# Kernel tuning notes

Hardware: AMD Instinct MI355X
Metric: run time of the kernel (lower is better)

Reference implementation:

```python
import jax, jax.numpy as jnp
import numpy as np

N_NODES = 50000
N_FEAT = 128
HIDDEN = 3
N_EDGES = 600000
N_POWERS = 3


def setup_inputs() -> dict:
    key = jax.random.key(0)
    ks = jax.random.split(key, 6)
    x = jax.random.normal(ks[0], (N_NODES, N_FEAT), dtype=jnp.float32)
    edge_index = jax.random.randint(ks[1], (N_POWERS, 2, N_EDGES), 0, N_NODES, dtype=jnp.int64)
    # MLP params for the 3 adjacency powers, stacked on the leading axis.
    # torch Linear(in,out) stored transposed here: y = x @ W + b.
    Wa = jax.random.normal(ks[2], (N_POWERS, N_FEAT, HIDDEN), dtype=jnp.float32) * (1.0 / np.sqrt(N_FEAT))
    ba = jax.random.normal(ks[3], (N_POWERS, HIDDEN), dtype=jnp.float32) * 0.01
    Wb = jax.random.normal(ks[4], (N_POWERS, HIDDEN, 1), dtype=jnp.float32) * (1.0 / np.sqrt(HIDDEN))
    bb = jax.random.normal(ks[5], (N_POWERS, 1), dtype=jnp.float32) * 0.01
    return {"x": x, "edge_index": edge_index, "Wa": Wa, "ba": ba, "Wb": Wb, "bb": bb}


def reference(x, edge_index, Wa, ba, Wb, bb):
    # Gather source/target node features per edge, per adjacency power.
    x_j = x[edge_index[:, 0]]          # [P, E, F]
    x_i = x[edge_index[:, 1]]          # [P, E, F]
    abs_dif = jnp.abs(x_j - x_i)       # [P, E, F]
    # Tiny per-edge MLP: Linear -> ReLU -> Linear -> Sigmoid (separate params per power).
    h = jax.nn.relu(jnp.einsum('pef,pfh->peh', abs_dif, Wa) + ba[:, None, :])  # [P, E, H]
    w = jax.nn.sigmoid(jnp.einsum('peh,pho->peo', h, Wb) + bb[:, None, :])     # [P, E, 1]
    return w[..., 0]                   # [P, E] edge weights for each power
```

## Files before the change

### kernel.cpp

```cpp
#include <hip/hip_runtime.h>
#include <math.h>

#define N_NODES 50000
#define N_FEAT  128
#define N_EDGES 600000
#define N_POWERS 3

#define PAIRS 5
#define EDGES_PER_BLK (64 * PAIRS)

#define CAP 81920
#define NBUCK 8
#define CHUNK 2048
#define NCHUNK 293

typedef _Float16 half2v __attribute__((ext_vector_type(2)));
union HU { unsigned u; half2v h; };

__device__ __forceinline__ int bucket_of(int j) { return (int)(((unsigned)j * 41u) >> 18); }

__device__ __forceinline__ unsigned long long match8(int b, bool valid) {
    const unsigned long long m0 = __ballot(b & 1);
    const unsigned long long m1 = __ballot(b & 2);
    const unsigned long long m2 = __ballot(b & 4);
    const unsigned long long vm = __ballot(valid);
    unsigned long long m = (b & 1) ? m0 : ~m0;
    m &= (b & 2) ? m1 : ~m1;
    m &= (b & 4) ? m2 : ~m2;
    return m & vm;
}

__global__ __launch_bounds__(256) void conv_x_plain(const float* __restrict__ x,
                                                    unsigned* __restrict__ xh,
                                                    const float* __restrict__ Wa,
                                                    unsigned* __restrict__ wah) {
    const int t = blockIdx.x * 256 + threadIdx.x;
    const float4* x4 = (const float4*)x;
    float4 a = x4[(size_t)t * 2];
    float4 b = x4[(size_t)t * 2 + 1];
    HU p0, p1, p2, p3;
    p0.h = half2v{(_Float16)a.x, (_Float16)a.y};
    p1.h = half2v{(_Float16)a.z, (_Float16)a.w};
    p2.h = half2v{(_Float16)b.x, (_Float16)b.y};
    p3.h = half2v{(_Float16)b.z, (_Float16)b.w};
    ((uint4*)xh)[t] = uint4{p0.u, p1.u, p2.u, p3.u};
    if (blockIdx.x == 0 && threadIdx.x < 192) {
        const int tt = threadIdx.x;
        #pragma unroll
        for (int q = 0; q < 3; ++q) {
            int idx = tt + q * 192;
            int c  = idx % 3;
            int pk = idx / 3;
            int k  = pk % 64;
            int p  = pk / 64;
            float w0 = Wa[p * 384 + (2 * k) * 3 + c];
            float w1 = Wa[p * 384 + (2 * k + 1) * 3 + c];
            HU u; u.h = half2v{(_Float16)w0, (_Float16)w1};
            wah[idx] = u.u;
        }
    }
}

__global__ __launch_bounds__(256) void hist_kernel(const int* __restrict__ edge_index,
                                                   int* __restrict__ hist) {
    __shared__ int lh[NBUCK];
    const int p = blockIdx.y, chunk = blockIdx.x;
    if (threadIdx.x < NBUCK) lh[threadIdx.x] = 0;
    __syncthreads();
    const int* ej = edge_index + (size_t)p * 2 * N_EDGES;
    const int base = chunk * CHUNK;
    const int lane = threadIdx.x & 63;
    #pragma unroll
    for (int k = 0; k < 8; ++k) {
        const int e = base + k * 256 + threadIdx.x;
        const bool valid = e < N_EDGES;
        const int j = __builtin_nontemporal_load(ej + (valid ? e : 0));
        const int b = bucket_of(j);
        const unsigned long long m = match8(b, valid);
        if (valid && lane == (int)__builtin_ctzll(m))
            atomicAdd(&lh[b], (int)__popcll(m));
    }
    __syncthreads();
    if (threadIdx.x < NBUCK)
        hist[(p * NBUCK + threadIdx.x) * NCHUNK + chunk] = lh[threadIdx.x];
}

__global__ __launch_bounds__(64) void scan_hist(int* __restrict__ hist,
                                                int* __restrict__ cur) {
    const int pb = blockIdx.x;
    const int lane = threadIdx.x;
    int* h = hist + pb * NCHUNK;
    int carry = 0;
    for (int t = 0; t < NCHUNK; t += 64) {
        const int c = t + lane;
        int v = (c < NCHUNK) ? h[c] : 0;
        int s = v;
        #pragma unroll
        for (int d = 1; d < 64; d <<= 1) {
            int u = __shfl_up(s, d, 64);
            if (lane >= d) s += u;
        }
        if (c < NCHUNK) h[c] = carry + (s - v);
        carry += __shfl(s, 63, 64);
    }
    if (lane == 0) cur[pb] = carry;
}

__global__ __launch_bounds__(256) void scatter_pass(const int* __restrict__ edge_index,
                                                    const int* __restrict__ hist,
                                                    unsigned long long* __restrict__ su) {
    __shared__ int lc[NBUCK];
    const int p = blockIdx.y, chunk = blockIdx.x;
    if (threadIdx.x < NBUCK)
        lc[threadIdx.x] = hist[(p * NBUCK + threadIdx.x) * NCHUNK + chunk];
    __syncthreads();
    const int* ej = edge_index + (size_t)p * 2 * N_EDGES;
    const int* ei = ej + N_EDGES;
    const int base = chunk * CHUNK;
    const int lane = threadIdx.x & 63;
    #pragma unroll
    for (int k = 0; k < 8; ++k) {
        const int e = base + k * 256 + threadIdx.x;
        const bool valid = e < N_EDGES;
        const int j = __builtin_nontemporal_load(ej + (valid ? e : 0));
        const int i = __builtin_nontemporal_load(ei + (valid ? e : 0));
        const int b = bucket_of(j);
        const unsigned long long m = match8(b, valid);
        const int ldr = m ? (int)__builtin_ctzll(m) : 0;
        int basepos = 0;
        if (valid && lane == ldr)
            basepos = atomicAdd(&lc[b], (int)__popcll(m));
        basepos = __shfl(basepos, ldr, 64);
        if (valid) {
            const int rank = (int)__popcll(m & ((1ull << lane) - 1ull));
            const size_t slot = (size_t)(p * NBUCK + b) * CAP + basepos + rank;
            su[slot] = (unsigned long long)(unsigned)(j | (i << 16))
                     | ((unsigned long long)e << 32);
        }
    }
}

template<int PAT>
__device__ __forceinline__ float swz(float v) {
    return __int_as_float(__builtin_amdgcn_ds_swizzle(__float_as_int(v), PAT));
}

__device__ __forceinline__ void dot3_8(const uint4& qa0, const uint4& qa1,
                                       const uint4& qb0, const uint4& qb1,
                                       const HU wa[8][3],
                                       float& h0, float& h1, float& h2) {
    unsigned ua[8] = {qa0.x, qa0.y, qa0.z, qa0.w, qa1.x, qa1.y, qa1.z, qa1.w};
    unsigned ub[8] = {qb0.x, qb0.y, qb0.z, qb0.w, qb1.x, qb1.y, qb1.z, qb1.w};
    h0 = 0.f; h1 = 0.f; h2 = 0.f;
    #pragma unroll
    for (int k = 0; k < 8; ++k) {
        HU a, b, d;
        a.u = ua[k]; b.u = ub[k];
        d.h = a.h - b.h;
        d.u &= 0x7fff7fffu;
        h0 = __builtin_amdgcn_fdot2(d.h, wa[k][0].h, h0, false);
        h1 = __builtin_amdgcn_fdot2(d.h, wa[k][1].h, h1, false);
        h2 = __builtin_amdgcn_fdot2(d.h, wa[k][2].h, h2, false);
    }
}

__global__ __launch_bounds__(256, 4) void adj_kernel_sorted(
    const unsigned* __restrict__ xh,
    const unsigned long long* __restrict__ su,
    const int* __restrict__ cur,
    const unsigned* __restrict__ wah,
    const float* __restrict__ ba,
    const float* __restrict__ Wb,
    const float* __restrict__ bb,
    float* __restrict__ out)
{
    const int p    = blockIdx.y;
    const int b    = blockIdx.x & 7;
    const int k    = blockIdx.x >> 3;
    const int tid  = threadIdx.x;
    const int lane = tid & 63;
    const int wave = tid >> 6;
    const int sub  = lane & 7;
    const int grp  = lane >> 3;

    const int count = cur[p * NBUCK + b];
    const int base  = k * EDGES_PER_BLK;
    if (base >= count) return;

    HU wa[8][3];
    {
        const unsigned* wp = wah + ((size_t)p * 64 + sub * 8) * 3;
        #pragma unroll
        for (int kk = 0; kk < 8; ++kk) {
            wa[kk][0].u = wp[kk * 3 + 0];
            wa[kk][1].u = wp[kk * 3 + 1];
            wa[kk][2].u = wp[kk * 3 + 2];
        }
        #pragma unroll
        for (int kk = 0; kk < 8; ++kk) {
            asm volatile("" : "+v"(wa[kk][0].u), "+v"(wa[kk][1].u), "+v"(wa[kk][2].u));
        }
    }

    const float ba0 = ba[p * 3 + 0], ba1 = ba[p * 3 + 1], ba2 = ba[p * 3 + 2];
    const float wb0 = Wb[p * 3 + 0], wb1 = Wb[p * 3 + 1], wb2 = Wb[p * 3 + 2];
    const float bbp = bb[p];

    const unsigned long long* sup = su + (size_t)(p * NBUCK + b) * CAP;
    float* outp = out + (size_t)p * N_EDGES;

    const int eoff = wave * 8 + grp;
    const int roff = sub * 8;
    const int cm1  = count - 1;

    unsigned long long q[2 * PAIRS];
    #pragma unroll
    for (int it = 0; it < PAIRS; ++it) {
        const int r1 = base + it * 64 + eoff;
        q[2 * it]     = __builtin_nontemporal_load(sup + min(r1, cm1));
        q[2 * it + 1] = __builtin_nontemporal_load(sup + min(r1 + 32, cm1));
    }

    uint4 A0, A1, B0, B1, C0, C1, D0, D1;
    {
        const int j1 = (int)(q[0] & 0xFFFFu), i1 = (int)((q[0] >> 16) & 0xFFFFu);
        const int j2 = (int)(q[1] & 0xFFFFu), i2 = (int)((q[1] >> 16) & 0xFFFFu);
        const uint4* rj1 = (const uint4*)(xh + ((size_t)j1 << 6) + roff);
        const uint4* ri1 = (const uint4*)(xh + ((size_t)i1 << 6) + roff);
        const uint4* rj2 = (const uint4*)(xh + ((size_t)j2 << 6) + roff);
        const uint4* ri2 = (const uint4*)(xh + ((size_t)i2 << 6) + roff);
        A0 = rj1[0]; A1 = rj1[1]; B0 = ri1[0]; B1 = ri1[1];
        C0 = rj2[0]; C1 = rj2[1]; D0 = ri2[0]; D1 = ri2[1];
    }

    #pragma unroll
    for (int it = 0; it < PAIRS; ++it) {
        uint4 nA0, nA1, nB0, nB1, nC0, nC1, nD0, nD1;
        if (it + 1 < PAIRS) {
            const int j1 = (int)(q[2 * it + 2] & 0xFFFFu), i1 = (int)((q[2 * it + 2] >> 16) & 0xFFFFu);
            const int j2 = (int)(q[2 * it + 3] & 0xFFFFu), i2 = (int)((q[2 * it + 3] >> 16) & 0xFFFFu);
            const uint4* rj1 = (const uint4*)(xh + ((size_t)j1 << 6) + roff);
            const uint4* ri1 = (const uint4*)(xh + ((size_t)i1 << 6) + roff);
            const uint4* rj2 = (const uint4*)(xh + ((size_t)j2 << 6) + roff);
            const uint4* ri2 = (const uint4*)(xh + ((size_t)i2 << 6) + roff);
            nA0 = rj1[0]; nA1 = rj1[1]; nB0 = ri1[0]; nB1 = ri1[1];
            nC0 = rj2[0]; nC1 = rj2[1]; nD0 = ri2[0]; nD1 = ri2[1];
        }

        float h0a, h1a, h2a, h0b, h1b, h2b;
        dot3_8(A0, A1, B0, B1, wa, h0a, h1a, h2a);
        dot3_8(C0, C1, D0, D1, wa, h0b, h1b, h2b);

        h0a += swz<0x041F>(h0a); h1a += swz<0x041F>(h1a); h2a += swz<0x041F>(h2a);
        h0b += swz<0x041F>(h0b); h1b += swz<0x041F>(h1b); h2b += swz<0x041F>(h2b);
        h0a += swz<0x081F>(h0a); h1a += swz<0x081F>(h1a); h2a += swz<0x081F>(h2a);
        h0b += swz<0x081F>(h0b); h1b += swz<0x081F>(h1b); h2b += swz<0x081F>(h2b);
        h0a += swz<0x101F>(h0a); h1a += swz<0x101F>(h1a); h2a += swz<0x101F>(h2a);
        h0b += swz<0x101F>(h0b); h1b += swz<0x101F>(h1b); h2b += swz<0x101F>(h2b);

        if (sub == 0) {
            const int r1 = base + it * 64 + eoff;
            const int r2 = r1 + 32;
            if (r1 < count) {
                const int e1 = (int)(q[2 * it] >> 32);
                float r0  = fmaxf(h0a + ba0, 0.f);
                float r1f = fmaxf(h1a + ba1, 0.f);
                float r2f = fmaxf(h2a + ba2, 0.f);
                float s   = fmaf(r0, wb0, fmaf(r1f, wb1, fmaf(r2f, wb2, bbp)));
                __builtin_nontemporal_store(1.f / (1.f + __expf(-s)), outp + e1);
            }
            if (r2 < count) {
                const int e2 = (int)(q[2 * it + 1] >> 32);
                float r0  = fmaxf(h0b + ba0, 0.f);
                float r1f = fmaxf(h1b + ba1, 0.f);
                float r2f = fmaxf(h2b + ba2, 0.f);
                float s   = fmaf(r0, wb0, fmaf(r1f, wb1, fmaf(r2f, wb2, bbp)));
                __builtin_nontemporal_store(1.f / (1.f + __expf(-s)), outp + e2);
            }
        }

        if (it + 1 < PAIRS) {
            A0 = nA0; A1 = nA1; B0 = nB0; B1 = nB1;
            C0 = nC0; C1 = nC1; D0 = nD0; D1 = nD1;
        }
    }
}

__global__ __launch_bounds__(256) void adj_kernel_f16(
    const unsigned* __restrict__ xh,
    const unsigned* __restrict__ wah,
    const int*   __restrict__ edge_index,
    const float* __restrict__ ba,
    const float* __restrict__ Wb,
    const float* __restrict__ bb,
    float* __restrict__ out)
{
    const int p    = blockIdx.y;
    const int tid  = threadIdx.x;
    const int lane = tid & 63;
    const int wave = tid >> 6;
    const int sub  = lane & 7;
    const int grp  = lane >> 3;

    HU wa[8][3];
    {
        const unsigned* wp = wah + ((size_t)p * 64 + sub * 8) * 3;
        #pragma unroll
        for (int k = 0; k < 8; ++k) {
            wa[k][0].u = wp[k * 3 + 0];
            wa[k][1].u = wp[k * 3 + 1];
            wa[k][2].u = wp[k * 3 + 2];
        }
        #pragma unroll
        for (int k = 0; k < 8; ++k) {
            asm volatile("" : "+v"(wa[k][0].u), "+v"(wa[k][1].u), "+v"(wa[k][2].u));
        }
    }

    const float ba0 = ba[p * 3 + 0], ba1 = ba[p * 3 + 1], ba2 = ba[p * 3 + 2];
    const float wb0 = Wb[p * 3 + 0], wb1 = Wb[p * 3 + 1], wb2 = Wb[p * 3 + 2];
    const float bbp = bb[p];

    const int* ej = edge_index + (size_t)p * 2 * N_EDGES;
    const int* ei = ej + N_EDGES;
    float* outp = out + (size_t)p * N_EDGES;

    const int e_blk = blockIdx.x * EDGES_PER_BLK;
    const int eoff  = wave * 8 + grp;
    const int roff  = sub * 8;

    #pragma unroll
    for (int it = 0; it < PAIRS; ++it) {
        const int e1 = e_blk + it * 64 + eoff;
        const int e2 = e1 + 32;
        const int j1 = __builtin_nontemporal_load(ej + e1);
        const int i1 = __builtin_nontemporal_load(ei + e1);
        const int j2 = __builtin_nontemporal_load(ej + e2);
        const int i2 = __builtin_nontemporal_load(ei + e2);

        const uint4* rj1 = (const uint4*)(xh + ((size_t)j1 << 6) + roff);
        const uint4* ri1 = (const uint4*)(xh + ((size_t)i1 << 6) + roff);
        const uint4* rj2 = (const uint4*)(xh + ((size_t)j2 << 6) + roff);
        const uint4* ri2 = (const uint4*)(xh + ((size_t)i2 << 6) + roff);
        uint4 a0 = rj1[0], a1 = rj1[1];
        uint4 b0 = ri1[0], b1 = ri1[1];
        uint4 c0 = rj2[0], c1 = rj2[1];
        uint4 d0 = ri2[0], d1 = ri2[1];

        float h0a, h1a, h2a, h0b, h1b, h2b;
        dot3_8(a0, a1, b0, b1, wa, h0a, h1a, h2a);
        dot3_8(c0, c1, d0, d1, wa, h0b, h1b, h2b);

        h0a += swz<0x041F>(h0a); h1a += swz<0x041F>(h1a); h2a += swz<0x041F>(h2a);
        h0b += swz<0x041F>(h0b); h1b += swz<0x041F>(h1b); h2b += swz<0x041F>(h2b);
        h0a += swz<0x081F>(h0a); h1a += swz<0x081F>(h1a); h2a += swz<0x081F>(h2a);
        h0b += swz<0x081F>(h0b); h1b += swz<0x081F>(h1b); h2b += swz<0x081F>(h2b);
        h0a += swz<0x101F>(h0a); h1a += swz<0x101F>(h1a); h2a += swz<0x101F>(h2a);
        h0b += swz<0x101F>(h0b); h1b += swz<0x101F>(h1b); h2b += swz<0x101F>(h2b);

        if (sub == 0) {
            float r0 = fmaxf(h0a + ba0, 0.f);
            float r1 = fmaxf(h1a + ba1, 0.f);
            float r2 = fmaxf(h2a + ba2, 0.f);
            float s  = fmaf(r0, wb0, fmaf(r1, wb1, fmaf(r2, wb2, bbp)));
            __builtin_nontemporal_store(1.f / (1.f + __expf(-s)), outp + e1);
            r0 = fmaxf(h0b + ba0, 0.f);
            r1 = fmaxf(h1b + ba1, 0.f);
            r2 = fmaxf(h2b + ba2, 0.f);
            s  = fmaf(r0, wb0, fmaf(r1, wb1, fmaf(r2, wb2, bbp)));
            __builtin_nontemporal_store(1.f / (1.f + __expf(-s)), outp + e2);
        }
    }
}

__global__ __launch_bounds__(256) void adj_kernel_f32(
    const float* __restrict__ x,
    const int*   __restrict__ edge_index,
    const float* __restrict__ Wa,
    const float* __restrict__ ba,
    const float* __restrict__ Wb,
    const float* __restrict__ bb,
    float* __restrict__ out)
{
    const int p    = blockIdx.y;
    const int tid  = threadIdx.x;
    const int lane = tid & 63;
    const int wave = tid >> 6;
    const int sub  = lane & 15;
    const int grp  = lane >> 4;
    const int f0 = sub * 8;

    const float* Wap = Wa + (size_t)p * N_FEAT * 3;
    float wa0[8], wa1[8], wa2[8];
    #pragma unroll
    for (int k = 0; k < 8; ++k) {
        wa0[k] = Wap[(f0 + k) * 3 + 0];
        wa1[k] = Wap[(f0 + k) * 3 + 1];
        wa2[k] = Wap[(f0 + k) * 3 + 2];
    }
    const float ba0 = ba[p * 3 + 0], ba1 = ba[p * 3 + 1], ba2 = ba[p * 3 + 2];
    const float wb0 = Wb[p * 3 + 0], wb1 = Wb[p * 3 + 1], wb2 = Wb[p * 3 + 2];
    const float bbp = bb[p];

    const int e = blockIdx.x * 16 + wave * 4 + grp;
    const int* ej = edge_index + (size_t)p * 2 * N_EDGES;
    const int* ei = ej + N_EDGES;
    const int j = ej[e];
    const int i = ei[e];

    const float4* xj = (const float4*)(x + (size_t)j * N_FEAT + f0);
    const float4* xi = (const float4*)(x + (size_t)i * N_FEAT + f0);
    float4 a0 = xj[0], a1 = xj[1];
    float4 b0 = xi[0], b1 = xi[1];

    float d[8];
    d[0] = fabsf(a0.x - b0.x); d[1] = fabsf(a0.y - b0.y);
    d[2] = fabsf(a0.z - b0.z); d[3] = fabsf(a0.w - b0.w);
    d[4] = fabsf(a1.x - b1.x); d[5] = fabsf(a1.y - b1.y);
    d[6] = fabsf(a1.z - b1.z); d[7] = fabsf(a1.w - b1.w);

    float h0 = 0.f, h1 = 0.f, h2 = 0.f;
    #pragma unroll
    for (int k = 0; k < 8; ++k) {
        h0 = fmaf(d[k], wa0[k], h0);
        h1 = fmaf(d[k], wa1[k], h1);
        h2 = fmaf(d[k], wa2[k], h2);
    }
    #pragma unroll
    for (int m = 1; m < 16; m <<= 1) {
        h0 += __shfl_xor(h0, m, 64);
        h1 += __shfl_xor(h1, m, 64);
        h2 += __shfl_xor(h2, m, 64);
    }
    if (sub == 0) {
        float r0 = fmaxf(h0 + ba0, 0.f);
        float r1 = fmaxf(h1 + ba1, 0.f);
        float r2 = fmaxf(h2 + ba2, 0.f);
        float s  = fmaf(r0, wb0, fmaf(r1, wb1, fmaf(r2, wb2, bbp)));
        float w  = 1.f / (1.f + expf(-s));
        out[(size_t)p * N_EDGES + e] = w;
    }
}

extern "C" void kernel_launch(void* const* d_in, const int* in_sizes, int n_in,
                              void* d_out, int out_size, void* d_ws, size_t ws_size,
                              hipStream_t stream) {
    const float* x          = (const float*)d_in[0];
    const int*   edge_index = (const int*)d_in[1];
    const float* Wa         = (const float*)d_in[2];
    const float* ba         = (const float*)d_in[3];
    const float* Wb         = (const float*)d_in[4];
    const float* bb         = (const float*)d_in[5];
    float* out = (float*)d_out;

    const size_t x_bytes    = (size_t)N_NODES * N_FEAT * 2;
    const size_t su_bytes   = (size_t)N_POWERS * NBUCK * CAP * 8;
    const size_t wa_bytes   = 2304;
    const size_t hist_bytes = (size_t)N_POWERS * NBUCK * NCHUNK * 4;
    const size_t cur_bytes  = NBUCK * N_POWERS * 4;
    const size_t need_full  = x_bytes + su_bytes + wa_bytes + hist_bytes + cur_bytes;

    if (ws_size >= need_full) {
        char* w = (char*)d_ws;
        unsigned* xh = (unsigned*)w;
        unsigned long long* su = (unsigned long long*)(w + x_bytes);
        unsigned* wah = (unsigned*)(w + x_bytes + su_bytes);
        int* hist = (int*)(w + x_bytes + su_bytes + wa_bytes);
        int* cur  = (int*)(w + x_bytes + su_bytes + wa_bytes + hist_bytes);

        conv_x_plain<<<N_NODES * N_FEAT / 2048, 256, 0, stream>>>(x, xh, Wa, wah);
        hist_kernel<<<dim3(NCHUNK, N_POWERS), 256, 0, stream>>>(edge_index, hist);
        scan_hist<<<NBUCK * N_POWERS, 64, 0, stream>>>(hist, cur);
        scatter_pass<<<dim3(NCHUNK, N_POWERS), 256, 0, stream>>>(edge_index, hist, su);
        dim3 grid(NBUCK * (CAP / EDGES_PER_BLK), N_POWERS);
        adj_kernel_sorted<<<grid, 256, 0, stream>>>(xh, su, cur, wah, ba, Wb, bb, out);
    } else if (ws_size >= x_bytes + wa_bytes) {
        unsigned* xh  = (unsigned*)d_ws;
        unsigned* wah = (unsigned*)((char*)d_ws + x_bytes);
        conv_x_plain<<<N_NODES * N_FEAT / 2048, 256, 0, stream>>>(x, xh, Wa, wah);
        dim3 grid(N_EDGES / EDGES_PER_BLK, N_POWERS);
        adj_kernel_f16<<<grid, 256, 0, stream>>>(xh, wah, edge_index, ba, Wb, bb, out);
    } else {
        dim3 grid((N_EDGES + 15) / 16, N_POWERS);
        adj_kernel_f32<<<grid, 256, 0, stream>>>(x, edge_index, Wa, ba, Wb, bb, out);
    }
}
```

Baseline: 175.0 us.

## Replace three-kernel bucket sort with single-pass 2D bucket scatter via global atomics

Swaps the histogram, scan and scatter kernels for one scatter kernel. It ranks edges locally in shared memory, reserves each chunk's slots with one global atomic per bucket, and writes coalesced runs to the output. Buckets become 64 two-dimensional bins over (j, i) node ranges instead of 8 bins over j, so the gather kernel touches a smaller set of both source and target rows. The price is a nondeterministic edge order within buckets, a larger shared memory footprint, and a fixed 10240-slot capacity per bucket that could overflow on skewed inputs.

```diff
diff --git a/kernel.cpp b/kernel.cpp
--- a/kernel.cpp
+++ b/kernel.cpp
@@ -9,31 +9,21 @@
 #define PAIRS 5
 #define EDGES_PER_BLK (64 * PAIRS)
 
-#define CAP 81920
-#define NBUCK 8
+#define NB64 64
+#define CAP64 10240
 #define CHUNK 2048
 #define NCHUNK 293
 
 typedef _Float16 half2v __attribute__((ext_vector_type(2)));
 union HU { unsigned u; half2v h; };
 
-__device__ __forceinline__ int bucket_of(int j) { return (int)(((unsigned)j * 41u) >> 18); }
-
-__device__ __forceinline__ unsigned long long match8(int b, bool valid) {
-    const unsigned long long m0 = __ballot(b & 1);
-    const unsigned long long m1 = __ballot(b & 2);
-    const unsigned long long m2 = __ballot(b & 4);
-    const unsigned long long vm = __ballot(valid);
-    unsigned long long m = (b & 1) ? m0 : ~m0;
-    m &= (b & 2) ? m1 : ~m1;
-    m &= (b & 4) ? m2 : ~m2;
-    return m & vm;
-}
+__device__ __forceinline__ int bj_of(int j) { return j / 6250; }
 
 __global__ __launch_bounds__(256) void conv_x_plain(const float* __restrict__ x,
                                                     unsigned* __restrict__ xh,
                                                     const float* __restrict__ Wa,
-                                                    unsigned* __restrict__ wah) {
+                                                    unsigned* __restrict__ wah,
+                                                    int* __restrict__ cur) {
     const int t = blockIdx.x * 256 + threadIdx.x;
     const float4* x4 = (const float4*)x;
     float4 a = x4[(size_t)t * 2];
@@ -59,84 +49,109 @@
             wah[idx] = u.u;
         }
     }
-}
-
-__global__ __launch_bounds__(256) void hist_kernel(const int* __restrict__ edge_index,
-                                                   int* __restrict__ hist) {
-    __shared__ int lh[NBUCK];
+    if (cur != nullptr && blockIdx.x == 1 && threadIdx.x < N_POWERS * NB64)
+        cur[threadIdx.x] = 0;
+}
+
+__global__ __launch_bounds__(256) void scatter_onepass(const int* __restrict__ edge_index,
+                                                       unsigned long long* __restrict__ su,
+                                                       int* __restrict__ cur) {
+    __shared__ int tot[4][NB64];
+    __shared__ int sh_w[4][NB64];
+    __shared__ int sh_lbase[NB64];
+    __shared__ int sh_delta[NB64];
+    __shared__ int sh_vt;
+    __shared__ unsigned long long pay[CHUNK];
+    __shared__ int dlt[CHUNK];
+
     const int p = blockIdx.y, chunk = blockIdx.x;
-    if (threadIdx.x < NBUCK) lh[threadIdx.x] = 0;
+    const int tid  = threadIdx.x;
+    const int lane = tid & 63;
+    const int wave = tid >> 6;
+    const int* ej = edge_index + (size_t)p * 2 * N_EDGES;
+    const int* ei = ej + N_EDGES;
+    const int base = chunk * CHUNK;
+
+    int jj[8], ii[8], sbk[8], off[8];
+    int run = 0;
+    #pragma unroll
+    for (int k = 0; k < 8; ++k) {
+        const int e = base + k * 256 + tid;
+        const bool valid = e < N_EDGES;
+        jj[k] = __builtin_nontemporal_load(ej + (valid ? e : 0));
+        ii[k] = __builtin_nontemporal_load(ei + (valid ? e : 0));
+        const int b = bj_of(jj[k]) * 8 + bj_of(ii[k]);
+        sbk[k] = b;
+        const unsigned long long m0 = __ballot(b & 1);
+        const unsigned long long m1 = __ballot(b & 2);
+        const unsigned long long m2 = __ballot(b & 4);
+        const unsigned long long m3 = __ballot(b & 8);
+        const unsigned long long m4 = __ballot(b & 16);
+        const unsigned long long m5 = __ballot(b & 32);
+        const unsigned long long vm = __ballot(valid);
+        unsigned long long m = ((b & 1) ? m0 : ~m0);
+        m &= ((b & 2)  ? m1 : ~m1);
+        m &= ((b & 4)  ? m2 : ~m2);
+        m &= ((b & 8)  ? m3 : ~m3);
+        m &= ((b & 16) ? m4 : ~m4);
+        m &= ((b & 32) ? m5 : ~m5);
+        m &= vm;
+        const int rank = (int)__popcll(m & ((1ull << lane) - 1ull));
+        unsigned long long mm = ((lane & 1) ? m0 : ~m0);
+        mm &= ((lane & 2)  ? m1 : ~m1);
+        mm &= ((lane & 4)  ? m2 : ~m2);
+        mm &= ((lane & 8)  ? m3 : ~m3);
+        mm &= ((lane & 16) ? m4 : ~m4);
+        mm &= ((lane & 32) ? m5 : ~m5);
+        mm &= vm;
+        const int cnt = (int)__popcll(mm);
+        const int pre = __shfl(run, b, 64);
+        off[k] = pre + rank;
+        run += cnt;
+    }
+    tot[wave][lane] = run;
     __syncthreads();
-    const int* ej = edge_index + (size_t)p * 2 * N_EDGES;
-    const int base = chunk * CHUNK;
-    const int lane = threadIdx.x & 63;
-    #pragma unroll
-    for (int k = 0; k < 8; ++k) {
-        const int e = base + k * 256 + threadIdx.x;
-        const bool valid = e < N_EDGES;
-        const int j = __builtin_nontemporal_load(ej + (valid ? e : 0));
-        const int b = bucket_of(j);
-        const unsigned long long m = match8(b, valid);
-        if (valid && lane == (int)__builtin_ctzll(m))
-            atomicAdd(&lh[b], (int)__popcll(m));
-    }
-    __syncthreads();
-    if (threadIdx.x < NBUCK)
-        hist[(p * NBUCK + threadIdx.x) * NCHUNK + chunk] = lh[threadIdx.x];
-}
-
-__global__ __launch_bounds__(64) void scan_hist(int* __restrict__ hist,
-                                                int* __restrict__ cur) {
-    const int pb = blockIdx.x;
-    const int lane = threadIdx.x;
-    int* h = hist + pb * NCHUNK;
-    int carry = 0;
-    for (int t = 0; t < NCHUNK; t += 64) {
-        const int c = t + lane;
-        int v = (c < NCHUNK) ? h[c] : 0;
-        int s = v;
+
+    if (tid < NB64) {
+        const int t0 = tot[0][tid], t1 = tot[1][tid], t2 = tot[2][tid], t3 = tot[3][tid];
+        const int bt = t0 + t1 + t2 + t3;
+        int s = bt;
         #pragma unroll
         for (int d = 1; d < 64; d <<= 1) {
             int u = __shfl_up(s, d, 64);
-            if (lane >= d) s += u;
-        }
-        if (c < NCHUNK) h[c] = carry + (s - v);
-        carry += __shfl(s, 63, 64);
-    }
-    if (lane == 0) cur[pb] = carry;
-}
-
-__global__ __launch_bounds__(256) void scatter_pass(const int* __restrict__ edge_index,
-                                                    const int* __restrict__ hist,
-                                                    unsigned long long* __restrict__ su) {
-    __shared__ int lc[NBUCK];
-    const int p = blockIdx.y, chunk = blockIdx.x;
-    if (threadIdx.x < NBUCK)
-        lc[threadIdx.x] = hist[(p * NBUCK + threadIdx.x) * NCHUNK + chunk];
+            if (tid >= d) s += u;
+        }
+        const int lb = s - bt;
+        const int g  = atomicAdd(&cur[p * NB64 + tid], bt);
+        sh_lbase[tid] = lb;
+        sh_delta[tid] = (p * NB64 + tid) * CAP64 + g - lb;
+        sh_w[0][tid] = 0;
+        sh_w[1][tid] = t0;
+        sh_w[2][tid] = t0 + t1;
+        sh_w[3][tid] = t0 + t1 + t2;
+        if (tid == 63) sh_vt = lb + bt;
+    }
     __syncthreads();
-    const int* ej = edge_index + (size_t)p * 2 * N_EDGES;
-    const int* ei = ej + N_EDGES;
-    const int base = chunk * CHUNK;
-    const int lane = threadIdx.x & 63;
+
     #pragma unroll
     for (int k = 0; k < 8; ++k) {
-        const int e = base + k * 256 + threadIdx.x;
-        const bool valid = e < N_EDGES;
-        const int j = __builtin_nontemporal_load(ej + (valid ? e : 0));
-        const int i = __builtin_nontemporal_load(ei + (valid ? e : 0));
-        const int b = bucket_of(j);
-        const unsigned long long m = match8(b, valid);
-        const int ldr = m ? (int)__builtin_ctzll(m) : 0;
-        int basepos = 0;
-        if (valid && lane == ldr)
-            basepos = atomicAdd(&lc[b], (int)__popcll(m));
-        basepos = __shfl(basepos, ldr, 64);
-        if (valid) {
-            const int rank = (int)__popcll(m & ((1ull << lane) - 1ull));
-            const size_t slot = (size_t)(p * NBUCK + b) * CAP + basepos + rank;
-            su[slot] = (unsigned long long)(unsigned)(j | (i << 16))
+        const int e = base + k * 256 + tid;
+        if (e < N_EDGES) {
+            const int b = sbk[k];
+            const int pos = sh_lbase[b] + sh_w[wave][b] + off[k];
+            pay[pos] = (unsigned long long)(unsigned)(jj[k] | (ii[k] << 16))
                      | ((unsigned long long)e << 32);
-        }
+            dlt[pos] = sh_delta[b];
+        }
+    }
+    __syncthreads();
+
+    const int vt = sh_vt;
+    #pragma unroll
+    for (int k = 0; k < 8; ++k) {
+        const int pos = k * 256 + tid;
+        if (pos < vt)
+            su[(size_t)(dlt[pos] + pos)] = pay[pos];
     }
 }
 
@@ -175,15 +190,17 @@
     float* __restrict__ out)
 {
     const int p    = blockIdx.y;
-    const int b    = blockIdx.x & 7;
-    const int k    = blockIdx.x >> 3;
+    const int bj   = blockIdx.x & 7;
+    const int k    = (blockIdx.x >> 3) & 31;
+    const int bi   = blockIdx.x >> 8;
+    const int sb   = bj * 8 + bi;
     const int tid  = threadIdx.x;
     const int lane = tid & 63;
     const int wave = tid >> 6;
     const int sub  = lane & 7;
     const int grp  = lane >> 3;
 
-    const int count = cur[p * NBUCK + b];
+    const int count = cur[p * NB64 + sb];
     const int base  = k * EDGES_PER_BLK;
     if (base >= count) return;
 
@@ -206,7 +223,7 @@
     const float wb0 = Wb[p * 3 + 0], wb1 = Wb[p * 3 + 1], wb2 = Wb[p * 3 + 2];
     const float bbp = bb[p];
 
-    const unsigned long long* sup = su + (size_t)(p * NBUCK + b) * CAP;
+    const unsigned long long* sup = su + (size_t)(p * NB64 + sb) * CAP64;
     float* outp = out + (size_t)p * N_EDGES;
 
     const int eoff = wave * 8 + grp;
@@ -454,30 +471,26 @@
     float* out = (float*)d_out;
 
     const size_t x_bytes    = (size_t)N_NODES * N_FEAT * 2;
-    const size_t su_bytes   = (size_t)N_POWERS * NBUCK * CAP * 8;
+    const size_t su_bytes   = (size_t)N_POWERS * NB64 * CAP64 * 8;
     const size_t wa_bytes   = 2304;
-    const size_t hist_bytes = (size_t)N_POWERS * NBUCK * NCHUNK * 4;
-    const size_t cur_bytes  = NBUCK * N_POWERS * 4;
-    const size_t need_full  = x_bytes + su_bytes + wa_bytes + hist_bytes + cur_bytes;
+    const size_t cur_bytes  = N_POWERS * NB64 * 4;
+    const size_t need_full  = x_bytes + su_bytes + wa_bytes + cur_bytes;
 
     if (ws_size >= need_full) {
         char* w = (char*)d_ws;
         unsigned* xh = (unsigned*)w;
         unsigned long long* su = (unsigned long long*)(w + x_bytes);
         unsigned* wah = (unsigned*)(w + x_bytes + su_bytes);
-        int* hist = (int*)(w + x_bytes + su_bytes + wa_bytes);
-        int* cur  = (int*)(w + x_bytes + su_bytes + wa_bytes + hist_bytes);
-
-        conv_x_plain<<<N_NODES * N_FEAT / 2048, 256, 0, stream>>>(x, xh, Wa, wah);
-        hist_kernel<<<dim3(NCHUNK, N_POWERS), 256, 0, stream>>>(edge_index, hist);
-        scan_hist<<<NBUCK * N_POWERS, 64, 0, stream>>>(hist, cur);
-        scatter_pass<<<dim3(NCHUNK, N_POWERS), 256, 0, stream>>>(edge_index, hist, su);
-        dim3 grid(NBUCK * (CAP / EDGES_PER_BLK), N_POWERS);
+        int* cur  = (int*)(w + x_bytes + su_bytes + wa_bytes);
+
+        conv_x_plain<<<N_NODES * N_FEAT / 2048, 256, 0, stream>>>(x, xh, Wa, wah, cur);
+        scatter_onepass<<<dim3(NCHUNK, N_POWERS), 256, 0, stream>>>(edge_index, su, cur);
+        dim3 grid(NB64 * (CAP64 / EDGES_PER_BLK), N_POWERS);
         adj_kernel_sorted<<<grid, 256, 0, stream>>>(xh, su, cur, wah, ba, Wb, bb, out);
     } else if (ws_size >= x_bytes + wa_bytes) {
         unsigned* xh  = (unsigned*)d_ws;
         unsigned* wah = (unsigned*)((char*)d_ws + x_bytes);
-        conv_x_plain<<<N_NODES * N_FEAT / 2048, 256, 0, stream>>>(x, xh, Wa, wah);
+        conv_x_plain<<<N_NODES * N_FEAT / 2048, 256, 0, stream>>>(x, xh, Wa, wah, nullptr);
         dim3 grid(N_EDGES / EDGES_PER_BLK, N_POWERS);
         adj_kernel_f16<<<grid, 256, 0, stream>>>(xh, wah, edge_index, ba, Wb, bb, out);
     } else {
```

After: 179.8 us. 2.8% more time.
